# Optimization experiments

Hardware: AMD Instinct MI355X
Metric: run time of the kernel (lower is better)

The kernel has to match this reference:

```python
import jax, jax.numpy as jnp
import numpy as np

ANCHORS = np.array([[10,13],[16,30],[33,23],[30,61],[62,45],[59,119],[116,90],[156,198],[373,326]], dtype=np.float32)
ANCHOR_MASK = [[6,7,8],[3,4,5],[0,1,2]]
CLASS_NUM = 80
IGNORE_THRESH = 0.5


def _bce_mean(z, x):
    # Keras BinaryCrossentropy(from_logits=True) called as a loss object:
    # elementwise sigmoid-CE, mean over last axis, then SUM_OVER_BATCH_SIZE
    # reduction == mean over ALL elements -> scalar.
    ce = jnp.maximum(x, 0.0) - x * z + jnp.log1p(jnp.exp(-jnp.abs(x)))
    return jnp.mean(ce)


def _layer_loss(out, lab, anchors):
    B, gh, gw, _ = out.shape
    A = anchors.shape[0]
    feats = out.reshape(B, gh, gw, A, CLASS_NUM + 5)
    anchors = jnp.asarray(anchors, dtype=jnp.float32)  # [A,2] (w,h)
    inp_wh = jnp.array([gw * 32, gh * 32], dtype=jnp.float32)  # reverse(input_shape)
    grid_wh = jnp.array([gw, gh], dtype=jnp.float32)           # reverse(grid_shape)

    gy, gx = jnp.meshgrid(jnp.arange(gh), jnp.arange(gw), indexing='ij')
    grid = jnp.stack([gx, gy], axis=-1).astype(jnp.float32)[:, :, None, :]  # [gh,gw,1,2]

    pred_xy = (jax.nn.sigmoid(feats[..., 0:2]) + grid) / grid_wh
    pred_wh = jnp.exp(feats[..., 2:4]) * anchors / inp_wh
    pred_box = jnp.concatenate([pred_xy, pred_wh], axis=-1)  # [B,gh,gw,A,4]

    obj = lab[..., 4:5]          # [B,gh,gw,A,1]
    objb = obj != 0.0
    N = gh * gw * A

    def _per_image(args):
        pb, tb, valid = args  # pb: [N,4] predicted, tb: [N,4] label boxes, valid: [N] bool
        b1_xy, b1_wh = pb[:, None, 0:2], pb[:, None, 2:4]
        b2_xy, b2_wh = tb[None, :, 0:2], tb[None, :, 2:4]
        b1_mins, b1_maxes = b1_xy - b1_wh / 2.0, b1_xy + b1_wh / 2.0
        b2_mins, b2_maxes = b2_xy - b2_wh / 2.0, b2_xy + b2_wh / 2.0
        inter_mins = jnp.maximum(b1_mins, b2_mins)
        inter_maxes = jnp.maximum(b1_maxes, b2_maxes)  # faithful to source (uses maximum, not minimum)
        inter_wh = jnp.maximum(inter_maxes - inter_mins, 0.0)
        inter = inter_wh[..., 0] * inter_wh[..., 1]
        a1 = b1_wh[..., 0] * b1_wh[..., 1]
        a2 = b2_wh[..., 0] * b2_wh[..., 1]
        iou = inter / (a1 + a2 - inter)  # [N,N]
        # only true boxes count; empty set -> best=-1 (matches tf reduce_max of empty = -inf)
        iou = jnp.where(valid[None, :], iou, -1.0)
        best_iou = jnp.max(iou, axis=-1)
        return (best_iou < IGNORE_THRESH).astype(jnp.float32)

    ignore = jax.lax.map(_per_image, (pred_box.reshape(B, N, 4),
                                      lab[..., 0:4].reshape(B, N, 4),
                                      objb.reshape(B, N)))
    ignore = jax.lax.stop_gradient(ignore).reshape(B, gh, gw, A, 1)

    raw_true_xy = lab[..., 0:2] * grid_wh - grid
    raw_true_wh = jnp.log(lab[..., 2:4] * inp_wh / anchors)
    raw_true_wh = jnp.where(objb, raw_true_wh, 0.0)
    box_loss_scale = 2.0 - lab[..., 2:3] * lab[..., 3:4]

    bf = jnp.float32(B)
    xy_loss = jnp.sum(obj * box_loss_scale * _bce_mean(raw_true_xy, feats[..., 0:2])) / bf
    wh_loss = jnp.sum(obj * box_loss_scale * 0.5 * jnp.square(raw_true_wh - feats[..., 2:4])) / bf
    conf_bce = _bce_mean(obj, feats[..., 4:5])
    conf_loss = jnp.sum(obj * conf_bce + (1.0 - obj) * conf_bce * ignore) / bf
    class_loss = jnp.sum(obj * _bce_mean(lab[..., 5:], feats[..., 5:])) / bf
    return xy_loss + wh_loss + conf_loss + class_loss


def _make_labels(key, B, g):
    k1, k2, k3, k4 = jax.random.split(key, 4)
    xy = jax.random.uniform(k1, (B, g, g, 3, 2), dtype=jnp.float32)
    wh = jax.random.uniform(k2, (B, g, g, 3, 2), dtype=jnp.float32, minval=0.05, maxval=1.0)
    objness = (jax.random.uniform(k3, (B, g, g, 3, 1)) < 0.02).astype(jnp.float32)
    cls = (jax.random.uniform(k4, (B, g, g, 3, CLASS_NUM)) < 0.05).astype(jnp.float32)
    return jnp.concatenate([xy, wh, objness, cls], axis=-1)


def setup_inputs() -> dict:
    key = jax.random.key(0)
    ks = jax.random.split(key, 6)
    B = 8
    grids = [13, 26, 52]
    out = {}
    for i, g in enumerate(grids):
        out[f'o{i}'] = jax.random.normal(ks[i], (B, g, g, 3 * (CLASS_NUM + 5)), dtype=jnp.float32)
        out[f'l{i}'] = _make_labels(ks[3 + i], B, g)
    return out


def reference(o0, o1, o2, l0, l1, l2):
    outputs = (o0, o1, o2)
    labels = (l0, l1, l2)
    loss = jnp.float32(0.0)
    for l in range(3):
        loss = loss + _layer_loss(outputs[l], labels[l], ANCHORS[ANCHOR_MASK[l]])
    return loss
```

## Files before the change

### kernel.cpp

```cpp
#include <hip/hip_runtime.h>
#include <math.h>

#define BDIM 256

__device__ __constant__ float c_aw[3][3] = {{116.f,156.f,373.f},{30.f,62.f,59.f},{10.f,16.f,33.f}};
__device__ __constant__ float c_ah[3][3] = {{90.f,198.f,326.f},{61.f,45.f,119.f},{13.f,30.f,23.f}};


__device__ __forceinline__ float bce_fast(float z, float x) {
    float t = __expf(-fabsf(x));
    return fmaxf(x, 0.f) - x * z + __logf(1.f + t);
}

__global__ __launch_bounds__(BDIM) void mega_a(
    const float* __restrict__ o0, const float* __restrict__ l0,
    const float* __restrict__ o1, const float* __restrict__ l1,
    const float* __restrict__ o2, const float* __restrict__ l2,
    double* __restrict__ acc, int* __restrict__ cnt, float4* __restrict__ tbox,
    float4* __restrict__ pbox, float* __restrict__ noobj)
{
    if (blockIdx.x < 1764) {
        int layer, blk0, nblk, n4;
        const float4 *O4, *L4;
        if (blockIdx.x < 84)       { layer=0; blk0=0;   nblk=84;   n4=86190;   O4=(const float4*)o0; L4=(const float4*)l0; }
        else if (blockIdx.x < 420) { layer=1; blk0=84;  nblk=336;  n4=344760;  O4=(const float4*)o1; L4=(const float4*)l1; }
        else                       { layer=2; blk0=420; nblk=1344; n4=1379040; O4=(const float4*)o2; L4=(const float4*)l2; }

        float s = 0.f;
        for (int i = (int)(blockIdx.x - blk0) * BDIM + (int)threadIdx.x; i < n4;
             i += nblk * BDIM) {
            float4 a = O4[i];
            float4 b = L4[i];
            s += bce_fast(b.x, a.x) + bce_fast(b.y, a.y)
               + bce_fast(b.z, a.z) + bce_fast(b.w, a.w);
        }
        __shared__ float sb[4];
        #pragma unroll
        for (int off = 32; off > 0; off >>= 1) s += __shfl_down(s, off, 64);
        if ((threadIdx.x & 63) == 0) sb[threadIdx.x >> 6] = s;
        __syncthreads();
        if (threadIdx.x == 0) {
            double t = (double)sb[0] + (double)sb[1] + (double)sb[2] + (double)sb[3];
            atomicAdd(&acc[layer * 8 + 0], t);
        }
        return;
    }

    int cb = blockIdx.x - 1764;
    int layer, blk0;
    if (cb < 16)      { layer = 0; blk0 = 0; }
    else if (cb < 80) { layer = 1; blk0 = 16; }
    else              { layer = 2; blk0 = 80; }
    const int g     = (layer == 0) ? 13 : (layer == 1) ? 26 : 52;
    const int Nlimg = g * g * 3;
    const int Cl    = 8 * Nlimg;
    const int cbase = (layer == 0) ? 0 : (layer == 1) ? 4056 : 20280;
    const float* O  = (layer == 0) ? o0 : (layer == 1) ? o1 : o2;
    const float* L  = (layer == 0) ? l0 : (layer == 1) ? l1 : l2;
    const float gf  = (float)g;
    const float inp = gf * 32.f;

    int cell = (cb - blk0) * BDIM + (int)threadIdx.x;
    float s_sub=0.f, s_xy=0.f, s_wh=0.f, s_conf=0.f, s_obj=0.f, s_s1=0.f;
    if (cell < Cl) {
        const float* op = O + (size_t)cell * 85;
        const float* lp = L + (size_t)cell * 85;
        float x0=op[0], x1=op[1], x2=op[2], x3=op[3], x4=op[4];
        float lx=lp[0], ly=lp[1], lw=lp[2], lh=lp[3], lobj=lp[4];
        int a  = cell % 3;
        int xi = (cell / 3) % g;
        int yi = (cell / (3 * g)) % g;
        int b  = cell / Nlimg;
        float aw = c_aw[layer][a], ah = c_ah[layer][a];

        float c4 = bce_fast(lobj, x4);
        s_sub  = bce_fast(lx,x0) + bce_fast(ly,x1)
               + bce_fast(lw,x2) + bce_fast(lh,x3) + c4;
        s_conf = c4;
        s_obj  = lobj;
        s_xy   = bce_fast(lx*gf - (float)xi, x0) + bce_fast(ly*gf - (float)yi, x1);

        float px = (1.f/(1.f+expf(-x0)) + (float)xi) / gf;
        float py = (1.f/(1.f+expf(-x1)) + (float)yi) / gf;
        float pw = expf(x2) * aw / inp;
        float ph = expf(x3) * ah / inp;
        pbox[cbase + cell]  = make_float4(px, py, pw, ph);
        noobj[cbase + cell] = 1.f - lobj;

        if (lobj != 0.f) {
            float bls = 2.f - lw * lh;
            s_s1 = lobj * bls;
            float dw = logf(lw * inp / aw) - x2;
            float dh = logf(lh * inp / ah) - x3;
            s_wh = lobj * bls * 0.5f * (dw * dw + dh * dh);
            int idx = atomicAdd(&cnt[layer * 8 + b], 1);
            tbox[cbase + b * Nlimg + idx] = make_float4(lx, ly, lw, lh);
        }
    }

    __shared__ float sb6[6][4];
    float v[6] = {s_sub, s_xy, s_wh, s_conf, s_obj, s_s1};
    #pragma unroll
    for (int q = 0; q < 6; q++) {
        float x = v[q];
        #pragma unroll
        for (int off = 32; off > 0; off >>= 1) x += __shfl_down(x, off, 64);
        if ((threadIdx.x & 63) == 0) sb6[q][threadIdx.x >> 6] = x;
    }
    __syncthreads();
    if (threadIdx.x < 6) {
        int q = threadIdx.x;
        double t = (double)sb6[q][0] + (double)sb6[q][1]
                 + (double)sb6[q][2] + (double)sb6[q][3];
        atomicAdd(&acc[layer * 8 + 1 + q], t);
    }
}

#define TCAP 512
__global__ __launch_bounds__(BDIM) void ignore_pass(
    double* __restrict__ acc, const int* __restrict__ cnt,
    const float4* __restrict__ tbox, const float4* __restrict__ pbox,
    const float* __restrict__ noobj)
{
    int layer, img, chunk;
    if (blockIdx.x < 16)      { layer = 0; img = blockIdx.x >> 1; chunk = blockIdx.x & 1; }
    else if (blockIdx.x < 80) { int t = blockIdx.x - 16; layer = 1; img = t >> 3; chunk = t & 7; }
    else                      { int t = blockIdx.x - 80; layer = 2; img = t >> 5; chunk = t & 31; }
    const int g     = (layer == 0) ? 13 : (layer == 1) ? 26 : 52;
    const int Nlimg = g * g * 3;
    const int cbase = (layer == 0) ? 0 : (layer == 1) ? 4056 : 20280;

    int ci = chunk * BDIM + (int)threadIdx.x;
    bool live = (ci < Nlimg);
    int cell = cbase + img * Nlimg + (live ? ci : 0);

    float pminx=0, pmaxx=0, pminy=0, pmaxy=0, a1=0, nb=0;
    if (live) {
        float4 p = pbox[cell];
        pminx = p.x - p.z*0.5f; pmaxx = p.x + p.z*0.5f;
        pminy = p.y - p.w*0.5f; pmaxy = p.y + p.w*0.5f;
        a1 = p.z * p.w;
        nb = noobj[cell];
    }
    int n = cnt[layer * 8 + img];
    const float4* tp = tbox + cbase + img * Nlimg;

    __shared__ float4 sT[TCAP];
    float best = -1.f;
    bool done = !live;
    for (int t0 = 0; t0 < n; t0 += TCAP) {
        int tn = min(TCAP, n - t0);
        __syncthreads();
        for (int i = threadIdx.x; i < tn; i += BDIM) sT[i] = tp[t0 + i];
        __syncthreads();
        if (!done) {
            for (int j = 0; j < tn; j++) {
                float4 t = sT[j];
                float hw = t.z*0.5f, hh = t.w*0.5f;
                float imnx = fmaxf(pminx, t.x - hw);
                float imxx = fmaxf(pmaxx, t.x + hw);
                float imny = fmaxf(pminy, t.y - hh);
                float imxy = fmaxf(pmaxy, t.y + hh);
                float iw = fmaxf(imxx - imnx, 0.f);
                float ih = fmaxf(imxy - imny, 0.f);
                float inter = iw * ih;
                float iou = inter / (a1 + t.z*t.w - inter);
                best = fmaxf(best, iou);
                if (best >= 0.5f) { done = true; break; }
            }
        }
    }
    float v = (live && best < 0.5f) ? nb : 0.f;

    __shared__ float sb[4];
    #pragma unroll
    for (int off = 32; off > 0; off >>= 1) v += __shfl_down(v, off, 64);
    if ((threadIdx.x & 63) == 0) sb[threadIdx.x >> 6] = v;
    __syncthreads();
    if (threadIdx.x == 0) {
        double t = (double)sb[0] + (double)sb[1] + (double)sb[2] + (double)sb[3];
        atomicAdd(&acc[layer * 8 + 7], t);
    }
}

__global__ void finalize_k(const double* __restrict__ acc, float* __restrict__ out)
{
    if (threadIdx.x == 0 && blockIdx.x == 0) {
        double loss = 0.0;
        const int gs[3] = {13, 26, 52};
        for (int l = 0; l < 3; l++) {
            double C   = 8.0 * gs[l] * gs[l] * 3.0;
            double S   = acc[l*8+0], sub = acc[l*8+1], xy = acc[l*8+2];
            double wh  = acc[l*8+3], cf  = acc[l*8+4], ob = acc[l*8+5];
            double s1  = acc[l*8+6], ni  = acc[l*8+7];
            double cls = (S - sub) / (C * 80.0);
            loss += ( (xy/(C*2.0))*s1 + wh + (cf/C)*(ob+ni) + cls*ob ) / 8.0;
        }
        out[0] = (float)loss;
    }
}

extern "C" void kernel_launch(void* const* d_in, const int* in_sizes, int n_in,
                              void* d_out, int out_size, void* d_ws, size_t ws_size,
                              hipStream_t stream)
{
    const float* o0 = (const float*)d_in[0];
    const float* l0 = (const float*)d_in[1];
    const float* o1 = (const float*)d_in[2];
    const float* l1 = (const float*)d_in[3];
    const float* o2 = (const float*)d_in[4];
    const float* l2 = (const float*)d_in[5];

    double* acc   = (double*)d_ws;
    int*    cnt   = (int*)((char*)d_ws + 192);
    float4* tbox  = (float4*)((char*)d_ws + 512);
    float4* pbox  = (float4*)((char*)d_ws + 1363328);
    float*  noobj = (float*)((char*)d_ws + 2726144);

    hipMemsetAsync(d_ws, 0, 512, stream);
    mega_a<<<2098, BDIM, 0, stream>>>(o0, l0, o1, l1, o2, l2,
                                      acc, cnt, tbox, pbox, noobj);
    ignore_pass<<<336, BDIM, 0, stream>>>(acc, cnt, tbox, pbox, noobj);
    finalize_k<<<1, 64, 0, stream>>>(acc, (float*)d_out);
}
```

Before: 150.5 us.

## Fuse finalize into ignore pass via last-block atomic; unroll BCE loop by two

```diff
diff --git a/kernel.cpp b/kernel.cpp
--- a/kernel.cpp
+++ b/kernel.cpp
@@ -10,6 +10,10 @@
 __device__ __forceinline__ float bce_fast(float z, float x) {
     float t = __expf(-fabsf(x));
     return fmaxf(x, 0.f) - x * z + __logf(1.f + t);
+}
+__device__ __forceinline__ float bce4(const float4& z, const float4& x) {
+    return bce_fast(z.x, x.x) + bce_fast(z.y, x.y)
+         + bce_fast(z.z, x.z) + bce_fast(z.w, x.w);
 }
 
 __global__ __launch_bounds__(BDIM) void mega_a(
@@ -26,14 +30,21 @@
         else if (blockIdx.x < 420) { layer=1; blk0=84;  nblk=336;  n4=344760;  O4=(const float4*)o1; L4=(const float4*)l1; }
         else                       { layer=2; blk0=420; nblk=1344; n4=1379040; O4=(const float4*)o2; L4=(const float4*)l2; }
 
-        float s = 0.f;
+        const int stride = nblk * BDIM;
+        float s0 = 0.f, s1 = 0.f;
         for (int i = (int)(blockIdx.x - blk0) * BDIM + (int)threadIdx.x; i < n4;
-             i += nblk * BDIM) {
+             i += 2 * stride) {
             float4 a = O4[i];
             float4 b = L4[i];
-            s += bce_fast(b.x, a.x) + bce_fast(b.y, a.y)
-               + bce_fast(b.z, a.z) + bce_fast(b.w, a.w);
-        }
+            int j = i + stride;
+            if (j < n4) {
+                float4 a2 = O4[j];
+                float4 b2 = L4[j];
+                s1 += bce4(b2, a2);
+            }
+            s0 += bce4(b, a);
+        }
+        float s = s0 + s1;
         __shared__ float sb[4];
         #pragma unroll
         for (int off = 32; off > 0; off >>= 1) s += __shfl_down(s, off, 64);
@@ -117,10 +128,12 @@
 }
 
 #define TCAP 512
-__global__ __launch_bounds__(BDIM) void ignore_pass(
+#define NB_IGNORE 336
+__global__ __launch_bounds__(BDIM) void ignore_fin(
     double* __restrict__ acc, const int* __restrict__ cnt,
     const float4* __restrict__ tbox, const float4* __restrict__ pbox,
-    const float* __restrict__ noobj)
+    const float* __restrict__ noobj, int* __restrict__ done,
+    float* __restrict__ out)
 {
     int layer, img, chunk;
     if (blockIdx.x < 16)      { layer = 0; img = blockIdx.x >> 1; chunk = blockIdx.x & 1; }
@@ -147,13 +160,13 @@
 
     __shared__ float4 sT[TCAP];
     float best = -1.f;
-    bool done = !live;
+    bool donef = !live;
     for (int t0 = 0; t0 < n; t0 += TCAP) {
         int tn = min(TCAP, n - t0);
         __syncthreads();
         for (int i = threadIdx.x; i < tn; i += BDIM) sT[i] = tp[t0 + i];
         __syncthreads();
-        if (!done) {
+        if (!donef) {
             for (int j = 0; j < tn; j++) {
                 float4 t = sT[j];
                 float hw = t.z*0.5f, hh = t.w*0.5f;
@@ -166,7 +179,7 @@
                 float inter = iw * ih;
                 float iou = inter / (a1 + t.z*t.w - inter);
                 best = fmaxf(best, iou);
-                if (best >= 0.5f) { done = true; break; }
+                if (best >= 0.5f) { donef = true; break; }
             }
         }
     }
@@ -180,23 +193,25 @@
     if (threadIdx.x == 0) {
         double t = (double)sb[0] + (double)sb[1] + (double)sb[2] + (double)sb[3];
         atomicAdd(&acc[layer * 8 + 7], t);
-    }
-}
-
-__global__ void finalize_k(const double* __restrict__ acc, float* __restrict__ out)
-{
-    if (threadIdx.x == 0 && blockIdx.x == 0) {
-        double loss = 0.0;
-        const int gs[3] = {13, 26, 52};
-        for (int l = 0; l < 3; l++) {
-            double C   = 8.0 * gs[l] * gs[l] * 3.0;
-            double S   = acc[l*8+0], sub = acc[l*8+1], xy = acc[l*8+2];
-            double wh  = acc[l*8+3], cf  = acc[l*8+4], ob = acc[l*8+5];
-            double s1  = acc[l*8+6], ni  = acc[l*8+7];
-            double cls = (S - sub) / (C * 80.0);
-            loss += ( (xy/(C*2.0))*s1 + wh + (cf/C)*(ob+ni) + cls*ob ) / 8.0;
-        }
-        out[0] = (float)loss;
+        __threadfence();
+        int old = atomicAdd(done, 1);
+        if (old == NB_IGNORE - 1) {
+            __threadfence();
+            double loss = 0.0;
+            const int gs[3] = {13, 26, 52};
+            for (int l = 0; l < 3; l++) {
+                double C = 8.0 * gs[l] * gs[l] * 3.0;
+                double q[8];
+                #pragma unroll
+                for (int k = 0; k < 8; k++)
+                    q[k] = __hip_atomic_load(&acc[l*8+k], __ATOMIC_RELAXED,
+                                             __HIP_MEMORY_SCOPE_AGENT);
+                double cls = (q[0] - q[1]) / (C * 80.0);
+                loss += ( (q[2]/(C*2.0))*q[6] + q[3]
+                        + (q[4]/C)*(q[5]+q[7]) + cls*q[5] ) / 8.0;
+            }
+            out[0] = (float)loss;
+        }
     }
 }
 
@@ -213,6 +228,7 @@
 
     double* acc   = (double*)d_ws;
     int*    cnt   = (int*)((char*)d_ws + 192);
+    int*    done  = (int*)((char*)d_ws + 288);
     float4* tbox  = (float4*)((char*)d_ws + 512);
     float4* pbox  = (float4*)((char*)d_ws + 1363328);
     float*  noobj = (float*)((char*)d_ws + 2726144);
@@ -220,6 +236,6 @@
     hipMemsetAsync(d_ws, 0, 512, stream);
     mega_a<<<2098, BDIM, 0, stream>>>(o0, l0, o1, l1, o2, l2,
                                       acc, cnt, tbox, pbox, noobj);
-    ignore_pass<<<336, BDIM, 0, stream>>>(acc, cnt, tbox, pbox, noobj);
-    finalize_k<<<1, 64, 0, stream>>>(acc, (float*)d_out);
-}
+    ignore_fin<<<NB_IGNORE, BDIM, 0, stream>>>(acc, cnt, tbox, pbox, noobj,
+                                               done, (float*)d_out);
+}
```

Measured after the change: 147.6 us. No clear change (-1.9%).
